# Kernel optimization log

Measured on AMD Instinct MI355X. Metric: run time of the kernel, lower is better.

## Reference

```python
import jax, jax.numpy as jnp
import numpy as np

NUM_NUM = 32    # numerical (pass-through) features
NUM_CAT = 32    # embedded categorical features
CARD = 128      # one-hot width per categorical feature
OUT = 32        # per-feature embedding output dim (0.25 * 128)
BATCH = 16384


def setup_inputs() -> dict:
    key = jax.random.key(0)
    k1, k2, k3 = jax.random.split(key, 3)
    x = jax.random.normal(k1, (BATCH, NUM_NUM + NUM_CAT * CARD), dtype=jnp.float32)
    # stacked per-feature nn.Linear(CARD, OUT) weights/biases (all same shape)
    W = jax.random.normal(k2, (NUM_CAT, CARD, OUT), dtype=jnp.float32) / np.sqrt(CARD).astype(np.float32)
    b = jax.random.normal(k3, (NUM_CAT, OUT), dtype=jnp.float32) * 0.01
    return {"x": x, "W": W, "b": b}


def reference(x, W, b):
    # Numerical columns pass through unchanged; each categorical one-hot slice
    # goes through its own small Linear, then everything is concatenated.
    # Since all categorical slices have identical width, the per-feature loop of
    # small GEMMs is expressed as one batched (block-diagonal) matmul.
    x_num = x[..., :NUM_NUM]                                      # [B, 32]
    x_cat = x[..., NUM_NUM:].reshape(x.shape[:-1] + (NUM_CAT, CARD))  # [B, F, C]
    emb = jnp.einsum('bfc,fco->bfo', x_cat, W) + b                # [B, F, OUT]
    emb = emb.reshape(x.shape[:-1] + (NUM_CAT * OUT,))            # [B, 1024]
    return jnp.concatenate([x_num, emb], axis=-1)                 # [B, 1056]
```

## Files before the change

### kernel.cpp

```cpp
#include <hip/hip_runtime.h>

#define BATCH   16384
#define NUM_NUM 32
#define NUM_CAT 32
#define CARD    128
#define OUT_F   32
#define XSTRIDE 4128
#define OSTRIDE 1056

#define TRB 64

typedef const __attribute__((address_space(1))) void* as1_cvp;
typedef __attribute__((address_space(3))) void*       as3_vp;

__global__ __launch_bounds__(256, 5) void emb_gemv(const float* __restrict__ x,
                                                   const float* __restrict__ Wm,
                                                   const float* __restrict__ bias,
                                                   float* __restrict__ out) {
    __shared__ float4 x_s[TRB * (CARD / 4)];

    const int f    = blockIdx.x;
    const int row0 = blockIdx.y * TRB;
    const int tid  = threadIdx.x;
    const int l    = tid & 63;
    const int lx   = l & 7;
    const int og   = __builtin_amdgcn_readfirstlane(tid >> 6);

    const float* xg = x + (size_t)row0 * XSTRIDE + NUM_NUM + f * CARD;

#pragma unroll
    for (int s = 0; s < 8; ++s) {
        const int i   = og * 8 + s;
        const int row = 2 * i + (l >> 5);
        const int cq  = (l & 31) ^ ((2 * i + (l >> 5)) & 7);
        __builtin_amdgcn_global_load_lds((as1_cvp)(xg + row * XSTRIDE + cq * 4),
                                         (as3_vp)&x_s[i * 64 + l], 16, 0, 0);
    }
    __syncthreads();

    const float4* __restrict__ wq =
        (const float4*)Wm + ((size_t)f * (CARD * OUT_F / 4) + og * 2);

    float acc[8];
#pragma unroll
    for (int k = 0; k < 8; ++k) acc[k] = 0.0f;

#pragma unroll 4
    for (int c4 = 0; c4 < CARD / 4; ++c4) {
        const float4 xv = x_s[l * 32 + (c4 ^ lx)];
#pragma unroll
        for (int cc = 0; cc < 4; ++cc) {
            const int    c  = c4 * 4 + cc;
            const float4 wa = wq[c * 8];
            const float4 wb = wq[c * 8 + 1];
            const float  xf = (&xv.x)[cc];
            acc[0] += xf * wa.x;  acc[1] += xf * wa.y;
            acc[2] += xf * wa.z;  acc[3] += xf * wa.w;
            acc[4] += xf * wb.x;  acc[5] += xf * wb.y;
            acc[6] += xf * wb.z;  acc[7] += xf * wb.w;
        }
    }
    __syncthreads();

#pragma unroll
    for (int k = 0; k < 2; ++k)
        x_s[l * 8 + ((og * 2 + k) ^ lx)] =
            make_float4(acc[k * 4], acc[k * 4 + 1], acc[k * 4 + 2], acc[k * 4 + 3]);
    __syncthreads();

#pragma unroll
    for (int p = 0; p < 2; ++p) {
        const int    r = p * 32 + (tid >> 3);
        const int    q = tid & 7;
        float4       v = x_s[r * 8 + (q ^ (r & 7))];
        const float4 b = ((const float4*)bias)[f * 8 + q];
        v.x += b.x; v.y += b.y; v.z += b.z; v.w += b.w;
        *(float4*)(out + (size_t)(row0 + r) * OSTRIDE + NUM_NUM + f * OUT_F + q * 4) = v;
    }

    if (f == 0) {
#pragma unroll
        for (int it = 0; it < 2; ++it) {
            const int idx = it * 256 + tid;
            const int r   = idx >> 3;
            const int c4  = (idx & 7) << 2;
            *(float4*)(out + (size_t)(row0 + r) * OSTRIDE + c4) =
                *(const float4*)(x + (size_t)(row0 + r) * XSTRIDE + c4);
        }
    }
}

extern "C" void kernel_launch(void* const* d_in, const int* in_sizes, int n_in,
                              void* d_out, int out_size, void* d_ws, size_t ws_size,
                              hipStream_t stream) {
    const float* x    = (const float*)d_in[0];
    const float* W    = (const float*)d_in[1];
    const float* bias = (const float*)d_in[2];
    float*       out  = (float*)d_out;

    dim3 grid(NUM_CAT, BATCH / TRB);
    emb_gemv<<<grid, 256, 0, stream>>>(x, W, bias, out);
}
```

Before: 92.82 us.

## Make each block own a row tile and double-buffer feature-pair loads through LDS

The grid changes from one block per (feature, row-tile) to one persistent 512-thread block per 64-row tile. That block iterates over 16 feature pairs, double-buffering async global-to-LDS loads of the next pair while it computes the current one. Bias add and output staging go through a separate LDS buffer, so each iteration writes fully coalesced 64-column output rows. This is meant to hide load latency inside a block and amortise launch and tail costs. In exchange the grid shrinks to 256 blocks with launch bounds (512,1), which lowers occupancy and may leave CUs underused, and correctness now depends on hand-written waitcnt and barrier placement.

New measurement: 260.7 us. +180.9%, slower.

```diff
diff --git a/kernel.cpp b/kernel.cpp
--- a/kernel.cpp
+++ b/kernel.cpp
@@ -9,84 +9,104 @@
 #define OSTRIDE 1056
 
 #define TRB 64
+#define NIT 16
+#define QPB (TRB * 64)
 
 typedef const __attribute__((address_space(1))) void* as1_cvp;
 typedef __attribute__((address_space(3))) void*       as3_vp;
 
-__global__ __launch_bounds__(256, 5) void emb_gemv(const float* __restrict__ x,
+__global__ __launch_bounds__(512, 1) void emb_pipe(const float* __restrict__ x,
                                                    const float* __restrict__ Wm,
                                                    const float* __restrict__ bias,
                                                    float* __restrict__ out) {
-    __shared__ float4 x_s[TRB * (CARD / 4)];
+    __shared__ float4 x_s[2][QPB];
+    __shared__ float4 ctr[TRB * 16];
 
-    const int f    = blockIdx.x;
-    const int row0 = blockIdx.y * TRB;
+    const int row0 = blockIdx.x * TRB;
     const int tid  = threadIdx.x;
     const int l    = tid & 63;
     const int lx   = l & 7;
-    const int og   = __builtin_amdgcn_readfirstlane(tid >> 6);
+    const int wv   = __builtin_amdgcn_readfirstlane(tid >> 6);
+    const int fsel = wv >> 2;
+    const int og   = wv & 3;
 
-    const float* xg = x + (size_t)row0 * XSTRIDE + NUM_NUM + f * CARD;
+    {
+        const int r  = tid >> 3;
+        const int c4 = (tid & 7) << 2;
+        *(float4*)(out + (size_t)(row0 + r) * OSTRIDE + c4) =
+            *(const float4*)(x + (size_t)(row0 + r) * XSTRIDE + c4);
+    }
 
+    const float* xbase = x + (size_t)row0 * XSTRIDE + NUM_NUM;
+
+    auto stage = [&](int item, int buf) {
+        const float* src0 = xbase + item * (2 * CARD);
 #pragma unroll
-    for (int s = 0; s < 8; ++s) {
-        const int i   = og * 8 + s;
-        const int row = 2 * i + (l >> 5);
-        const int cq  = (l & 31) ^ ((2 * i + (l >> 5)) & 7);
-        __builtin_amdgcn_global_load_lds((as1_cvp)(xg + row * XSTRIDE + cq * 4),
-                                         (as3_vp)&x_s[i * 64 + l], 16, 0, 0);
-    }
-    __syncthreads();
+        for (int s = 0; s < 8; ++s) {
+            const int i = wv * 8 + s;
+            __builtin_amdgcn_global_load_lds(
+                (as1_cvp)(src0 + (size_t)i * XSTRIDE + ((l ^ (i & 7)) << 2)),
+                (as3_vp)&x_s[buf][i * 64 + l], 16, 0, 0);
+        }
+    };
 
-    const float4* __restrict__ wq =
-        (const float4*)Wm + ((size_t)f * (CARD * OUT_F / 4) + og * 2);
+    stage(0, 0);
+    stage(1, 1);
 
-    float acc[8];
+    for (int it = 0; it < NIT; ++it) {
+        if (it < NIT - 1) { asm volatile("s_waitcnt vmcnt(8)" ::: "memory"); }
+        else              { asm volatile("s_waitcnt vmcnt(4)" ::: "memory"); }
+        __builtin_amdgcn_s_barrier();
+        __builtin_amdgcn_sched_barrier(0);
+
+        const float4* xb  = x_s[it & 1];
+        const float4* wqn = (const float4*)Wm +
+                            ((size_t)(it * 2 + fsel) * (CARD * OUT_F / 4) + og * 2);
+
+        float acc[8];
 #pragma unroll
-    for (int k = 0; k < 8; ++k) acc[k] = 0.0f;
+        for (int k = 0; k < 8; ++k) acc[k] = 0.0f;
 
 #pragma unroll 4
-    for (int c4 = 0; c4 < CARD / 4; ++c4) {
-        const float4 xv = x_s[l * 32 + (c4 ^ lx)];
+        for (int c4 = 0; c4 < 32; ++c4) {
+            const float4 xv = xb[l * 64 + fsel * 32 + (c4 ^ lx)];
 #pragma unroll
-        for (int cc = 0; cc < 4; ++cc) {
-            const int    c  = c4 * 4 + cc;
-            const float4 wa = wq[c * 8];
-            const float4 wb = wq[c * 8 + 1];
-            const float  xf = (&xv.x)[cc];
-            acc[0] += xf * wa.x;  acc[1] += xf * wa.y;
-            acc[2] += xf * wa.z;  acc[3] += xf * wa.w;
-            acc[4] += xf * wb.x;  acc[5] += xf * wb.y;
-            acc[6] += xf * wb.z;  acc[7] += xf * wb.w;
+            for (int cc = 0; cc < 4; ++cc) {
+                const int    c  = c4 * 4 + cc;
+                const float4 wa = wqn[c * 8];
+                const float4 wb = wqn[c * 8 + 1];
+                const float  xf = (&xv.x)[cc];
+                acc[0] += xf * wa.x;  acc[1] += xf * wa.y;
+                acc[2] += xf * wa.z;  acc[3] += xf * wa.w;
+                acc[4] += xf * wb.x;  acc[5] += xf * wb.y;
+                acc[6] += xf * wb.z;  acc[7] += xf * wb.w;
+            }
         }
-    }
-    __syncthreads();
 
-#pragma unroll
-    for (int k = 0; k < 2; ++k)
-        x_s[l * 8 + ((og * 2 + k) ^ lx)] =
-            make_float4(acc[k * 4], acc[k * 4 + 1], acc[k * 4 + 2], acc[k * 4 + 3]);
-    __syncthreads();
+        __builtin_amdgcn_s_barrier();
+        __builtin_amdgcn_sched_barrier(0);
+        if (it + 2 < NIT) stage(it + 2, it & 1);
 
-#pragma unroll
-    for (int p = 0; p < 2; ++p) {
-        const int    r = p * 32 + (tid >> 3);
-        const int    q = tid & 7;
-        float4       v = x_s[r * 8 + (q ^ (r & 7))];
-        const float4 b = ((const float4*)bias)[f * 8 + q];
-        v.x += b.x; v.y += b.y; v.z += b.z; v.w += b.w;
-        *(float4*)(out + (size_t)(row0 + r) * OSTRIDE + NUM_NUM + f * OUT_F + q * 4) = v;
-    }
+        const float4* bq = (const float4*)bias + ((it * 2 + fsel) * 8 + og * 2);
+        const float4  b0 = bq[0];
+        const float4  b1 = bq[1];
+        const int     cq0 = fsel * 8 + og * 2;
+        ctr[l * 16 + (cq0 ^ lx)] =
+            make_float4(acc[0] + b0.x, acc[1] + b0.y, acc[2] + b0.z, acc[3] + b0.w);
+        ctr[l * 16 + ((cq0 + 1) ^ lx)] =
+            make_float4(acc[4] + b1.x, acc[5] + b1.y, acc[6] + b1.z, acc[7] + b1.w);
 
-    if (f == 0) {
-#pragma unroll
-        for (int it = 0; it < 2; ++it) {
-            const int idx = it * 256 + tid;
-            const int r   = idx >> 3;
-            const int c4  = (idx & 7) << 2;
-            *(float4*)(out + (size_t)(row0 + r) * OSTRIDE + c4) =
-                *(const float4*)(x + (size_t)(row0 + r) * XSTRIDE + c4);
-        }
+        asm volatile("s_waitcnt lgkmcnt(0)" ::: "memory");
+        __builtin_amdgcn_s_barrier();
+        __builtin_amdgcn_sched_barrier(0);
+
+        const int    rr = tid >> 3;
+        const int    qp = (tid & 7) * 2;
+        const float4 v0 = ctr[rr * 16 + (qp ^ (rr & 7))];
+        const float4 v1 = ctr[rr * 16 + ((qp + 1) ^ (rr & 7))];
+        float* orow = out + (size_t)(row0 + rr) * OSTRIDE + NUM_NUM + it * 64 + qp * 4;
+        *(float4*)(orow)     = v0;
+        *(float4*)(orow + 4) = v1;
     }
 }
 
@@ -98,6 +118,5 @@
     const float* bias = (const float*)d_in[2];
     float*       out  = (float*)d_out;
 
-    dim3 grid(NUM_CAT, BATCH / TRB);
-    emb_gemv<<<grid, 256, 0, stream>>>(x, W, bias, out);
+    emb_pipe<<<BATCH / TRB / 1, 512, 0, stream>>>(x, W, bias, out);
 }
```

## Double-buffer x tile in K-chunks to overlap LDS loads with compute

Applied to the files above, without the earlier changes.

Splits the 128-wide categorical slice into four 32-column chunks staged into two LDS buffers via global_load_lds, so later chunks load while earlier ones are computed. This halves the LDS footprint per block and raises the launch-bounds occupancy hint from 5 to 6. Bias is now added before the LDS transpose, and each thread writes two float4s per row. The double buffering adds barriers per chunk, and it is unclear whether the first wait properly covers the outstanding async loads.

Result: faster. 87.50 us (-5.7%).

```diff
diff --git a/kernel.cpp b/kernel.cpp
--- a/kernel.cpp
+++ b/kernel.cpp
@@ -8,16 +8,19 @@
 #define XSTRIDE 4128
 #define OSTRIDE 1056
 
-#define TRB 64
+#define TRB    64
+#define CK     32
+#define NCHUNK (CARD / CK)
+#define QPB    (TRB * CK / 4)
 
 typedef const __attribute__((address_space(1))) void* as1_cvp;
 typedef __attribute__((address_space(3))) void*       as3_vp;
 
-__global__ __launch_bounds__(256, 5) void emb_gemv(const float* __restrict__ x,
+__global__ __launch_bounds__(256, 6) void emb_gemv(const float* __restrict__ x,
                                                    const float* __restrict__ Wm,
                                                    const float* __restrict__ bias,
                                                    float* __restrict__ out) {
-    __shared__ float4 x_s[TRB * (CARD / 4)];
+    __shared__ float4 lds[2 * QPB];
 
     const int f    = blockIdx.x;
     const int row0 = blockIdx.y * TRB;
@@ -26,17 +29,22 @@
     const int lx   = l & 7;
     const int og   = __builtin_amdgcn_readfirstlane(tid >> 6);
 
-    const float* xg = x + (size_t)row0 * XSTRIDE + NUM_NUM + f * CARD;
+    const float* xg   = x + (size_t)row0 * XSTRIDE + NUM_NUM + f * CARD;
+    const int    srow = l >> 3;
+    const int    scq  = (l & 7) ^ ((l >> 3) & 7);
 
+    auto stage = [&](int ck, int buf) {
 #pragma unroll
-    for (int s = 0; s < 8; ++s) {
-        const int i   = og * 8 + s;
-        const int row = 2 * i + (l >> 5);
-        const int cq  = (l & 31) ^ ((2 * i + (l >> 5)) & 7);
-        __builtin_amdgcn_global_load_lds((as1_cvp)(xg + row * XSTRIDE + cq * 4),
-                                         (as3_vp)&x_s[i * 64 + l], 16, 0, 0);
-    }
-    __syncthreads();
+        for (int s = 0; s < 2; ++s) {
+            const int i = og * 2 + s;
+            __builtin_amdgcn_global_load_lds(
+                (as1_cvp)(xg + (size_t)(i * 8 + srow) * XSTRIDE + ck * CK + scq * 4),
+                (as3_vp)&lds[buf * QPB + i * 64 + l], 16, 0, 0);
+        }
+    };
+
+    stage(0, 0);
+    stage(1, 1);
 
     const float4* __restrict__ wq =
         (const float4*)Wm + ((size_t)f * (CARD * OUT_F / 4) + og * 2);
@@ -45,37 +53,52 @@
 #pragma unroll
     for (int k = 0; k < 8; ++k) acc[k] = 0.0f;
 
-#pragma unroll 4
-    for (int c4 = 0; c4 < CARD / 4; ++c4) {
-        const float4 xv = x_s[l * 32 + (c4 ^ lx)];
+    __syncthreads();
+
+    for (int ck = 0; ck < NCHUNK; ++ck) {
+        const float4* xb = &lds[(ck & 1) * QPB];
+
+        float4 xv[8];
 #pragma unroll
-        for (int cc = 0; cc < 4; ++cc) {
-            const int    c  = c4 * 4 + cc;
-            const float4 wa = wq[c * 8];
-            const float4 wb = wq[c * 8 + 1];
-            const float  xf = (&xv.x)[cc];
-            acc[0] += xf * wa.x;  acc[1] += xf * wa.y;
-            acc[2] += xf * wa.z;  acc[3] += xf * wa.w;
-            acc[4] += xf * wb.x;  acc[5] += xf * wb.y;
-            acc[6] += xf * wb.z;  acc[7] += xf * wb.w;
+        for (int c4 = 0; c4 < 8; ++c4) xv[c4] = xb[l * 8 + (c4 ^ lx)];
+
+#pragma unroll
+        for (int c4 = 0; c4 < 8; ++c4) {
+#pragma unroll
+            for (int cc = 0; cc < 4; ++cc) {
+                const int    c  = ck * CK + c4 * 4 + cc;
+                const float4 wa = wq[c * 8];
+                const float4 wb = wq[c * 8 + 1];
+                const float  xf = (&xv[c4].x)[cc];
+                acc[0] += xf * wa.x;  acc[1] += xf * wa.y;
+                acc[2] += xf * wa.z;  acc[3] += xf * wa.w;
+                acc[4] += xf * wb.x;  acc[5] += xf * wb.y;
+                acc[6] += xf * wb.z;  acc[7] += xf * wb.w;
+            }
+        }
+
+        if (ck < NCHUNK - 1) {
+            __syncthreads();
+            if (ck + 2 < NCHUNK) stage(ck + 2, ck & 1);
         }
     }
+
+    const float4 b0 = ((const float4*)bias)[f * 8 + og * 2];
+    const float4 b1 = ((const float4*)bias)[f * 8 + og * 2 + 1];
+    lds[l * 8 + ((og * 2) ^ lx)] =
+        make_float4(acc[0] + b0.x, acc[1] + b0.y, acc[2] + b0.z, acc[3] + b0.w);
+    lds[l * 8 + ((og * 2 + 1) ^ lx)] =
+        make_float4(acc[4] + b1.x, acc[5] + b1.y, acc[6] + b1.z, acc[7] + b1.w);
     __syncthreads();
 
-#pragma unroll
-    for (int k = 0; k < 2; ++k)
-        x_s[l * 8 + ((og * 2 + k) ^ lx)] =
-            make_float4(acc[k * 4], acc[k * 4 + 1], acc[k * 4 + 2], acc[k * 4 + 3]);
-    __syncthreads();
-
-#pragma unroll
-    for (int p = 0; p < 2; ++p) {
-        const int    r = p * 32 + (tid >> 3);
-        const int    q = tid & 7;
-        float4       v = x_s[r * 8 + (q ^ (r & 7))];
-        const float4 b = ((const float4*)bias)[f * 8 + q];
-        v.x += b.x; v.y += b.y; v.z += b.z; v.w += b.w;
-        *(float4*)(out + (size_t)(row0 + r) * OSTRIDE + NUM_NUM + f * OUT_F + q * 4) = v;
+    {
+        const int    r  = tid >> 2;
+        const int    qp = (tid & 3) * 2;
+        const float4 v0 = lds[r * 8 + (qp ^ (r & 7))];
+        const float4 v1 = lds[r * 8 + ((qp + 1) ^ (r & 7))];
+        float* orow = out + (size_t)(row0 + r) * OSTRIDE + NUM_NUM + f * OUT_F + qp * 4;
+        *(float4*)(orow)     = v0;
+        *(float4*)(orow + 4) = v1;
     }
 
     if (f == 0) {
```

## Process feature pairs per block with double-buffered async LDS staging

Applied to the files above, without the earlier changes.

Each block now handles two categorical features instead of one, which halves the grid. The 256-column x slice is staged in 64-column chunks into two LDS buffers with global_load_lds, so the next chunk's loads overlap the current chunk's FMAs. Bias is added before the LDS transpose, and each output row is written as a contiguous 64-float span, giving wider stores. The cost is doubled LDS per block (32 KB), which may reduce occupancy, plus more barriers.

Measured after the change: 157.6 us. 1.7x slower.

```diff
diff --git a/kernel.cpp b/kernel.cpp
--- a/kernel.cpp
+++ b/kernel.cpp
@@ -13,72 +13,112 @@
 typedef const __attribute__((address_space(1))) void* as1_cvp;
 typedef __attribute__((address_space(3))) void*       as3_vp;
 
-__global__ __launch_bounds__(256, 5) void emb_gemv(const float* __restrict__ x,
+__global__ __launch_bounds__(256, 5) void emb_pair(const float* __restrict__ x,
                                                    const float* __restrict__ Wm,
                                                    const float* __restrict__ bias,
                                                    float* __restrict__ out) {
-    __shared__ float4 x_s[TRB * (CARD / 4)];
+    __shared__ float4 xs[2][1024];
 
-    const int f    = blockIdx.x;
+    const int p    = blockIdx.x;
     const int row0 = blockIdx.y * TRB;
     const int tid  = threadIdx.x;
     const int l    = tid & 63;
     const int lx   = l & 7;
     const int og   = __builtin_amdgcn_readfirstlane(tid >> 6);
 
-    const float* xg = x + (size_t)row0 * XSTRIDE + NUM_NUM + f * CARD;
+    const float* xg = x + (size_t)row0 * XSTRIDE + NUM_NUM + p * 256;
 
+    int soff[4];
 #pragma unroll
-    for (int s = 0; s < 8; ++s) {
-        const int i   = og * 8 + s;
-        const int row = 2 * i + (l >> 5);
-        const int cq  = (l & 31) ^ ((2 * i + (l >> 5)) & 7);
-        __builtin_amdgcn_global_load_lds((as1_cvp)(xg + row * XSTRIDE + cq * 4),
-                                         (as3_vp)&x_s[i * 64 + l], 16, 0, 0);
+    for (int s = 0; s < 4; ++s) {
+        const int i  = og * 4 + s;
+        const int sr = i * 4 + (l >> 4);
+        const int sq = (l & 15) ^ (sr & 7);
+        soff[s] = sr * XSTRIDE + sq * 4;
     }
+
+    auto stage = [&](int ck, int buf) {
+#pragma unroll
+        for (int s = 0; s < 4; ++s)
+            __builtin_amdgcn_global_load_lds((as1_cvp)(xg + ck * 64 + soff[s]),
+                                             (as3_vp)&xs[buf][(og * 4 + s) * 64 + l],
+                                             16, 0, 0);
+    };
+
+    float acc[2][8];
+#pragma unroll
+    for (int a = 0; a < 2; ++a)
+#pragma unroll
+        for (int k = 0; k < 8; ++k) acc[a][k] = 0.0f;
+
+    stage(0, 0);
+    stage(1, 1);
     __syncthreads();
 
-    const float4* __restrict__ wq =
-        (const float4*)Wm + ((size_t)f * (CARD * OUT_F / 4) + og * 2);
+    auto compute = [&](const float4* xb, int fs, int cb) {
+        const float4* wqf = (const float4*)Wm +
+                            ((size_t)(p * 2 + fs) * (CARD * OUT_F / 4) + og * 2);
+        float* a = acc[fs];
+#pragma unroll
+        for (int h = 0; h < 2; ++h) {
+            float4 xv[8];
+#pragma unroll
+            for (int k = 0; k < 8; ++k) xv[k] = xb[l * 16 + h * 8 + (k ^ lx)];
+#pragma unroll
+            for (int k = 0; k < 8; ++k) {
+#pragma unroll
+                for (int cc = 0; cc < 4; ++cc) {
+                    const int    c  = cb + h * 32 + k * 4 + cc;
+                    const float4 wa = wqf[c * 8];
+                    const float4 wb = wqf[c * 8 + 1];
+                    const float  xf = (&xv[k].x)[cc];
+                    a[0] += xf * wa.x;  a[1] += xf * wa.y;
+                    a[2] += xf * wa.z;  a[3] += xf * wa.w;
+                    a[4] += xf * wb.x;  a[5] += xf * wb.y;
+                    a[6] += xf * wb.z;  a[7] += xf * wb.w;
+                }
+            }
+        }
+    };
 
-    float acc[8];
+    compute(xs[0], 0, 0);
+    __syncthreads();
+    stage(2, 0);
+    compute(xs[1], 0, 64);
+    __syncthreads();
+    stage(3, 1);
+    compute(xs[0], 1, 0);
+    __syncthreads();
+    compute(xs[1], 1, 64);
+
+    float4* ctr = xs[0];
 #pragma unroll
-    for (int k = 0; k < 8; ++k) acc[k] = 0.0f;
+    for (int fs = 0; fs < 2; ++fs) {
+        const float4 b0 = ((const float4*)bias)[(p * 2 + fs) * 8 + og * 2];
+        const float4 b1 = ((const float4*)bias)[(p * 2 + fs) * 8 + og * 2 + 1];
+        const int    q0 = fs * 8 + og * 2;
+        ctr[l * 16 + (q0 ^ lx)] =
+            make_float4(acc[fs][0] + b0.x, acc[fs][1] + b0.y,
+                        acc[fs][2] + b0.z, acc[fs][3] + b0.w);
+        ctr[l * 16 + ((q0 + 1) ^ lx)] =
+            make_float4(acc[fs][4] + b1.x, acc[fs][5] + b1.y,
+                        acc[fs][6] + b1.z, acc[fs][7] + b1.w);
+    }
+    asm volatile("s_waitcnt lgkmcnt(0)" ::: "memory");
+    __builtin_amdgcn_s_barrier();
 
-#pragma unroll 4
-    for (int c4 = 0; c4 < CARD / 4; ++c4) {
-        const float4 xv = x_s[l * 32 + (c4 ^ lx)];
+    {
+        const int r  = tid >> 2;
+        const int q0 = (tid & 3) * 4;
+        float4 v[4];
 #pragma unroll
-        for (int cc = 0; cc < 4; ++cc) {
-            const int    c  = c4 * 4 + cc;
-            const float4 wa = wq[c * 8];
-            const float4 wb = wq[c * 8 + 1];
-            const float  xf = (&xv.x)[cc];
-            acc[0] += xf * wa.x;  acc[1] += xf * wa.y;
-            acc[2] += xf * wa.z;  acc[3] += xf * wa.w;
-            acc[4] += xf * wb.x;  acc[5] += xf * wb.y;
-            acc[6] += xf * wb.z;  acc[7] += xf * wb.w;
-        }
-    }
-    __syncthreads();
-
+        for (int j = 0; j < 4; ++j) v[j] = ctr[r * 16 + ((q0 + j) ^ (r & 7))];
+        float* orow = out + (size_t)(row0 + r) * OSTRIDE + NUM_NUM + p * 64 + q0 * 4;
 #pragma unroll
-    for (int k = 0; k < 2; ++k)
-        x_s[l * 8 + ((og * 2 + k) ^ lx)] =
-            make_float4(acc[k * 4], acc[k * 4 + 1], acc[k * 4 + 2], acc[k * 4 + 3]);
-    __syncthreads();
-
-#pragma unroll
-    for (int p = 0; p < 2; ++p) {
-        const int    r = p * 32 + (tid >> 3);
-        const int    q = tid & 7;
-        float4       v = x_s[r * 8 + (q ^ (r & 7))];
-        const float4 b = ((const float4*)bias)[f * 8 + q];
-        v.x += b.x; v.y += b.y; v.z += b.z; v.w += b.w;
-        *(float4*)(out + (size_t)(row0 + r) * OSTRIDE + NUM_NUM + f * OUT_F + q * 4) = v;
+        for (int j = 0; j < 4; ++j) *(float4*)(orow + j * 4) = v[j];
     }
 
-    if (f == 0) {
+    if (p == 0) {
 #pragma unroll
         for (int it = 0; it < 2; ++it) {
             const int idx = it * 256 + tid;
@@ -98,6 +138,6 @@
     const float* bias = (const float*)d_in[2];
     float*       out  = (float*)d_out;
 
-    dim3 grid(NUM_CAT, BATCH / TRB);
-    emb_gemv<<<grid, 256, 0, stream>>>(x, W, bias, out);
+    dim3 grid(NUM_CAT / 2, BATCH / TRB);
+    emb_pair<<<grid, 256, 0, stream>>>(x, W, bias, out);
 }
```
